# Kernel tuning notes

Measured on AMD Instinct MI355X. Metric: run time of the kernel, lower is better.

Reference implementation:

```python
import jax, jax.numpy as jnp
import numpy as np

D = 512  # input_channels
K = 64   # centers_num


def setup_inputs() -> dict:
    key = jax.random.key(0)
    k1, k2, k3, k4 = jax.random.split(key, 4)
    inputs = jax.random.normal(k1, (32, D, 56, 56), dtype=jnp.float32)
    # conv 1x1 weight/bias (nn.Conv2d(input_channels, centers_num, (1,1)))
    conv_w = jax.random.normal(k2, (K, D), dtype=jnp.float32) * (1.0 / np.sqrt(D))
    conv_b = jax.random.normal(k3, (K,), dtype=jnp.float32) * 0.01
    # centers ~ U(-0.1, 0.1), shape [D, K]
    centers = jax.random.uniform(k4, (D, K), dtype=jnp.float32, minval=-0.1, maxval=0.1)
    return {"inputs": inputs, "conv_w": conv_w, "conv_b": conv_b, "centers": centers}


def reference(inputs, conv_w, conv_b, centers):
    B, d, H, W = inputs.shape
    N = H * W
    x = inputs.reshape(B, d, N)                      # [B,D,N]
    # 1x1 conv == per-pixel linear: logits [B,K,N]
    logits = jnp.einsum('kd,bdn->bkn', conv_w, x) + conv_b[None, :, None]
    alpha = jax.nn.softmax(logits, axis=1)           # softmax over K (dim=1)
    # vlad[b,d,k] = sum_n alpha[b,k,n] * (x[b,d,n] - centers[d,k])
    vlad = jnp.einsum('bkn,bdn->bdk', alpha, x) - centers[None] * alpha.sum(axis=2)[:, None, :]
    # intra-normalize over D (torch.norm default p=2, no eps)
    vlad = vlad / jnp.linalg.norm(vlad, axis=1, keepdims=True)
    vlad = vlad.reshape(B, d * K)
    vlad = vlad / jnp.linalg.norm(vlad, axis=1, keepdims=True)
    return vlad
```

## Files before the change

### kernel.cpp

```cpp
#include <hip/hip_runtime.h>
#include <math.h>


#define NN 3136
#define DD 512
#define KK 64
#define BB 32

typedef short bf16x8 __attribute__((ext_vector_type(8)));
typedef float f32x4  __attribute__((ext_vector_type(4)));

#define SEL_HI   0x05040100u
#define SEL_LO   0x07060302u
#define SEL_PACK 0x07060302u

union FragU { uint4 u; bf16x8 f; };

static __device__ inline bf16x8 frag4(unsigned a, unsigned b, unsigned c, unsigned d) {
    FragU x; x.u = make_uint4(a, b, c, d); return x.f;
}

static __device__ inline unsigned short bf16_rne(float f) {
    unsigned u = __float_as_uint(f);
    return (unsigned short)((u + 0x7FFFu + ((u >> 16) & 1u)) >> 16);
}

__global__ __launch_bounds__(256) void wprep_kernel(
    const float* __restrict__ w, unsigned short* __restrict__ wh,
    unsigned short* __restrict__ wl, float* __restrict__ asum,
    float* __restrict__ vlad)
{
    const int i = blockIdx.x * 256 + threadIdx.x;
    if (i < 32768) {
        float v = w[i];
        float hif = __uint_as_float(__float_as_uint(v) & 0xFFFF0000u);
        float lof = v - hif;
        wh[i] = (unsigned short)(__float_as_uint(v) >> 16);
        wl[i] = (unsigned short)(__float_as_uint(lof) >> 16);
    }
    *(float4*)&vlad[(size_t)i * 4] = make_float4(0.f, 0.f, 0.f, 0.f);
    if (i < 2048) asum[i] = 0.f;
}

__global__ __launch_bounds__(256, 4) void fused_vlad(
    const float* __restrict__ x,
    const unsigned short* __restrict__ wh,
    const unsigned short* __restrict__ wl,
    const float* __restrict__ bias,
    float* __restrict__ asum,
    float* __restrict__ vlad)
{
    const int b  = blockIdx.y;
    const int n0 = blockIdx.x * 128;
    const int t  = threadIdx.x;
    const int lane = t & 63;
    const int wv   = t >> 6;
    const int c = lane & 15;
    const int q = lane >> 4;

    __shared__ __align__(16) unsigned xs_raw[128 * 36];
    __shared__ __align__(16) unsigned short wsh[64][40];
    __shared__ __align__(16) unsigned short wsl[64][40];
    unsigned short* as_ = (unsigned short*)xs_raw;

    f32x4 acc[4][2];
    #pragma unroll
    for (int mt = 0; mt < 4; mt++)
        #pragma unroll
        for (int r = 0; r < 4; r++) {
            float bv = bias[mt * 16 + q * 4 + r];
            acc[mt][0][r] = bv; acc[mt][1][r] = bv;
        }

    const float* xb = x + (size_t)b * DD * NN;
    const int n4 = t & 31;
    const int dr = t >> 5;
    const int wrow = t >> 2, wc8 = t & 3;

    float xr[16];
    uint4 wrh, wrl;
    {
        #pragma unroll
        for (int j = 0; j < 4; j++) {
            int nn = n0 + n4 + 32 * j;
            if (nn > NN - 1) nn = NN - 1;
            #pragma unroll
            for (int p = 0; p < 4; p++)
                xr[j * 4 + p] = xb[(size_t)(dr * 4 + p) * NN + nn];
        }
        wrh = *(const uint4*)&wh[(size_t)wrow * DD + wc8 * 8];
        wrl = *(const uint4*)&wl[(size_t)wrow * DD + wc8 * 8];
    }

    for (int dc = 0; dc < 16; dc++) {
        uint4 xp[4];
        #pragma unroll
        for (int j = 0; j < 4; j++) {
            unsigned pk[4];
            #pragma unroll
            for (int p = 0; p < 4; p++) {
                float v = xr[j * 4 + p];
                float hif = __uint_as_float(__float_as_uint(v) & 0xFFFF0000u);
                float lof = v - hif;
                pk[p] = __builtin_amdgcn_perm(__float_as_uint(lof), __float_as_uint(v), SEL_PACK);
            }
            xp[j] = make_uint4(pk[0], pk[1], pk[2], pk[3]);
        }
        uint4 wch = wrh, wcl = wrl;

        if (dc < 15) {
            const int d0 = (dc + 1) * 32;
            #pragma unroll
            for (int j = 0; j < 4; j++) {
                int nn = n0 + n4 + 32 * j;
                if (nn > NN - 1) nn = NN - 1;
                #pragma unroll
                for (int p = 0; p < 4; p++)
                    xr[j * 4 + p] = xb[(size_t)(d0 + dr * 4 + p) * NN + nn];
            }
            wrh = *(const uint4*)&wh[(size_t)wrow * DD + d0 + wc8 * 8];
            wrl = *(const uint4*)&wl[(size_t)wrow * DD + d0 + wc8 * 8];
        }

        __syncthreads();
        #pragma unroll
        for (int j = 0; j < 4; j++)
            *(uint4*)&xs_raw[(n4 + 32 * j) * 36 + dr * 4] = xp[j];
        *(uint4*)&wsh[wrow][wc8 * 8] = wch;
        *(uint4*)&wsl[wrow][wc8 * 8] = wcl;
        __syncthreads();

        bf16x8 ah[4], al[4], bh[2], bl[2];
        #pragma unroll
        for (int mt = 0; mt < 4; mt++) {
            ah[mt] = *(const bf16x8*)&wsh[mt * 16 + c][q * 8];
            al[mt] = *(const bf16x8*)&wsl[mt * 16 + c][q * 8];
        }
        #pragma unroll
        for (int nt = 0; nt < 2; nt++) {
            const int row = wv * 32 + nt * 16 + c;
            uint4 p0 = *(const uint4*)&xs_raw[row * 36 + q * 8];
            uint4 p1 = *(const uint4*)&xs_raw[row * 36 + q * 8 + 4];
            bh[nt] = frag4(__builtin_amdgcn_perm(p0.y, p0.x, SEL_HI),
                           __builtin_amdgcn_perm(p0.w, p0.z, SEL_HI),
                           __builtin_amdgcn_perm(p1.y, p1.x, SEL_HI),
                           __builtin_amdgcn_perm(p1.w, p1.z, SEL_HI));
            bl[nt] = frag4(__builtin_amdgcn_perm(p0.y, p0.x, SEL_LO),
                           __builtin_amdgcn_perm(p0.w, p0.z, SEL_LO),
                           __builtin_amdgcn_perm(p1.y, p1.x, SEL_LO),
                           __builtin_amdgcn_perm(p1.w, p1.z, SEL_LO));
        }
        #pragma unroll
        for (int mt = 0; mt < 4; mt++)
            #pragma unroll
            for (int nt = 0; nt < 2; nt++) {
                acc[mt][nt] = __builtin_amdgcn_mfma_f32_16x16x32_bf16(ah[mt], bh[nt], acc[mt][nt], 0, 0, 0);
                acc[mt][nt] = __builtin_amdgcn_mfma_f32_16x16x32_bf16(ah[mt], bl[nt], acc[mt][nt], 0, 0, 0);
                acc[mt][nt] = __builtin_amdgcn_mfma_f32_16x16x32_bf16(al[mt], bh[nt], acc[mt][nt], 0, 0, 0);
            }
    }

    __syncthreads();

    float sa[4][4];
    #pragma unroll
    for (int mt = 0; mt < 4; mt++)
        #pragma unroll
        for (int r = 0; r < 4; r++) sa[mt][r] = 0.f;

    #pragma unroll
    for (int nt = 0; nt < 2; nt++) {
        float mx = -1e30f;
        #pragma unroll
        for (int mt = 0; mt < 4; mt++)
            #pragma unroll
            for (int r = 0; r < 4; r++) mx = fmaxf(mx, acc[mt][nt][r]);
        mx = fmaxf(mx, __shfl_xor(mx, 16));
        mx = fmaxf(mx, __shfl_xor(mx, 32));
        float s = 0.f;
        #pragma unroll
        for (int mt = 0; mt < 4; mt++)
            #pragma unroll
            for (int r = 0; r < 4; r++) {
                float e = __expf(acc[mt][nt][r] - mx);
                acc[mt][nt][r] = e; s += e;
            }
        s += __shfl_xor(s, 16);
        s += __shfl_xor(s, 32);
        const float rinv = 1.0f / s;
        const int nloc = wv * 32 + nt * 16 + c;
        const bool ok = (n0 + nloc) < NN;
        #pragma unroll
        for (int mt = 0; mt < 4; mt++)
            #pragma unroll
            for (int r = 0; r < 4; r++) {
                unsigned short ub = bf16_rne(acc[mt][nt][r] * rinv);
                if (!ok) ub = 0;
                as_[(mt * 16 + q * 4 + r) * 136 + nloc] = ub;
                if (ok) sa[mt][r] += __uint_as_float((unsigned)ub << 16);
            }
    }
    #pragma unroll
    for (int off = 1; off <= 8; off <<= 1)
        #pragma unroll
        for (int mt = 0; mt < 4; mt++)
            #pragma unroll
            for (int r = 0; r < 4; r++)
                sa[mt][r] += __shfl_xor(sa[mt][r], off);
    if (c == 0) {
        #pragma unroll
        for (int mt = 0; mt < 4; mt++)
            #pragma unroll
            for (int r = 0; r < 4; r++)
                atomicAdd(&asum[b * KK + mt * 16 + q * 4 + r], sa[mt][r]);
    }

    __syncthreads();

    const float* xw = x + ((size_t)b * DD + wv * 128) * NN;
    float* pvb = vlad + ((size_t)b * DD + wv * 128) * KK;

    #pragma unroll
    for (int dh = 0; dh < 2; dh++) {
        f32x4 acc2[4][4];
        #pragma unroll
        for (int dt = 0; dt < 4; dt++)
            #pragma unroll
            for (int kt = 0; kt < 4; kt++)
                #pragma unroll
                for (int r = 0; r < 4; r++) acc2[dt][kt][r] = 0.f;

        #pragma unroll
        for (int ns = 0; ns < 4; ns++) {
            int nn = n0 + ns * 32 + q * 8;
            if (nn > NN - 8) nn = NN - 8;
            float4 xv[4][2];
            #pragma unroll
            for (int dt = 0; dt < 4; dt++) {
                const size_t ro = (size_t)(dh * 64 + dt * 16 + c) * NN;
                xv[dt][0] = *(const float4*)&xw[ro + nn];
                xv[dt][1] = *(const float4*)&xw[ro + nn + 4];
            }
            bf16x8 bfr[4];
            #pragma unroll
            for (int kt = 0; kt < 4; kt++)
                bfr[kt] = *(const bf16x8*)&as_[(kt * 16 + c) * 136 + ns * 32 + q * 8];
            #pragma unroll
            for (int dt = 0; dt < 4; dt++) {
                const float4 va = xv[dt][0], vb2 = xv[dt][1];
                unsigned ux = __float_as_uint(va.x),  uy = __float_as_uint(va.y);
                unsigned uz = __float_as_uint(va.z),  uw = __float_as_uint(va.w);
                unsigned vx = __float_as_uint(vb2.x), vy = __float_as_uint(vb2.y);
                unsigned vz = __float_as_uint(vb2.z), vw = __float_as_uint(vb2.w);
                bf16x8 ah = frag4(__builtin_amdgcn_perm(uy, ux, SEL_LO),
                                  __builtin_amdgcn_perm(uw, uz, SEL_LO),
                                  __builtin_amdgcn_perm(vy, vx, SEL_LO),
                                  __builtin_amdgcn_perm(vw, vz, SEL_LO));
                float lax = va.x - __uint_as_float(ux & 0xFFFF0000u);
                float lay = va.y - __uint_as_float(uy & 0xFFFF0000u);
                float laz = va.z - __uint_as_float(uz & 0xFFFF0000u);
                float law = va.w - __uint_as_float(uw & 0xFFFF0000u);
                float lbx = vb2.x - __uint_as_float(vx & 0xFFFF0000u);
                float lby = vb2.y - __uint_as_float(vy & 0xFFFF0000u);
                float lbz = vb2.z - __uint_as_float(vz & 0xFFFF0000u);
                float lbw = vb2.w - __uint_as_float(vw & 0xFFFF0000u);
                bf16x8 al2 = frag4(
                    __builtin_amdgcn_perm(__float_as_uint(lay), __float_as_uint(lax), SEL_LO),
                    __builtin_amdgcn_perm(__float_as_uint(law), __float_as_uint(laz), SEL_LO),
                    __builtin_amdgcn_perm(__float_as_uint(lby), __float_as_uint(lbx), SEL_LO),
                    __builtin_amdgcn_perm(__float_as_uint(lbw), __float_as_uint(lbz), SEL_LO));
                #pragma unroll
                for (int kt = 0; kt < 4; kt++) {
                    acc2[dt][kt] = __builtin_amdgcn_mfma_f32_16x16x32_bf16(ah,  bfr[kt], acc2[dt][kt], 0, 0, 0);
                    acc2[dt][kt] = __builtin_amdgcn_mfma_f32_16x16x32_bf16(al2, bfr[kt], acc2[dt][kt], 0, 0, 0);
                }
            }
        }
        #pragma unroll
        for (int dt = 0; dt < 4; dt++)
            #pragma unroll
            for (int r = 0; r < 4; r++) {
                const size_t dl = (size_t)(dh * 64 + dt * 16 + q * 4 + r) * KK;
                #pragma unroll
                for (int kt = 0; kt < 4; kt++)
                    atomicAdd(&pvb[dl + kt * 16 + c], acc2[dt][kt][r]);
            }
    }
}

__global__ __launch_bounds__(256) void combine_norm(
    const float* __restrict__ centers, const float* __restrict__ asum,
    float* __restrict__ vlad, float* __restrict__ psq)
{
    const int dchunk = blockIdx.x;
    const int b = blockIdx.y;
    const int t = threadIdx.x;
    const int k4 = (t & 15) * 4;
    const int dq = t >> 4;
    const float4 av = *(const float4*)&asum[b * KK + k4];
    float sqx = 0.f, sqy = 0.f, sqz = 0.f, sqw = 0.f;
    for (int i = 0; i < 8; i++) {
        const int d = dchunk * 128 + i * 16 + dq;
        const size_t idx = ((size_t)b * DD + d) * KK + k4;
        float4 p = *(const float4*)&vlad[idx];
        const float4 cv = *(const float4*)&centers[d * KK + k4];
        float vx = p.x - cv.x * av.x, vy = p.y - cv.y * av.y;
        float vz = p.z - cv.z * av.z, vw = p.w - cv.w * av.w;
        *(float4*)&vlad[idx] = make_float4(vx, vy, vz, vw);
        sqx = fmaf(vx, vx, sqx); sqy = fmaf(vy, vy, sqy);
        sqz = fmaf(vz, vz, sqz); sqw = fmaf(vw, vw, sqw);
    }
    __shared__ float red[16][64];
    red[dq][k4 + 0] = sqx; red[dq][k4 + 1] = sqy;
    red[dq][k4 + 2] = sqz; red[dq][k4 + 3] = sqw;
    __syncthreads();
    if (t < 64) {
        float s = 0.f;
        #pragma unroll
        for (int qq = 0; qq < 16; qq++) s += red[qq][t];
        psq[(b * 4 + dchunk) * 64 + t] = s;
    }
}

__global__ __launch_bounds__(256) void finalize_kernel(
    const float* __restrict__ psq, const float* __restrict__ vlad,
    float* __restrict__ out)
{
    const int dchunk = blockIdx.x;
    const int b = blockIdx.y;
    const int t = threadIdx.x;
    __shared__ float cn[64];
    if (t < 64) {
        float s = psq[b * 256 + t] + psq[b * 256 + 64 + t]
                + psq[b * 256 + 128 + t] + psq[b * 256 + 192 + t];
        cn[t] = 1.0f / (sqrtf(s) * 8.0f);
    }
    __syncthreads();
    const int k4 = (t & 15) * 4;
    const int dq = t >> 4;
    const float4 cv = *(const float4*)&cn[k4];
    #pragma unroll
    for (int i = 0; i < 8; i++) {
        const size_t idx = ((size_t)b * DD + dchunk * 128 + i * 16 + dq) * KK + k4;
        float4 v = *(const float4*)&vlad[idx];
        *(float4*)&out[idx] = make_float4(v.x * cv.x, v.y * cv.y, v.z * cv.z, v.w * cv.w);
    }
}

extern "C" void kernel_launch(void* const* d_in, const int* in_sizes, int n_in,
                              void* d_out, int out_size, void* d_ws, size_t ws_size,
                              hipStream_t stream) {
    const float* x       = (const float*)d_in[0];
    const float* conv_w  = (const float*)d_in[1];
    const float* conv_b  = (const float*)d_in[2];
    const float* centers = (const float*)d_in[3];
    float* out = (float*)d_out;

    unsigned short* wh = (unsigned short*)d_ws;
    unsigned short* wl = wh + 32768;
    float* asum = (float*)(wl + 32768);
    float* vlad = asum + 2048;
    float* psq  = vlad + 1048576;

    wprep_kernel   <<<dim3(1024),    dim3(256), 0, stream>>>(conv_w, wh, wl, asum, vlad);
    fused_vlad     <<<dim3(25, BB),  dim3(256), 0, stream>>>(x, wh, wl, conv_b, asum, vlad);
    combine_norm   <<<dim3(4, BB),   dim3(256), 0, stream>>>(centers, asum, vlad, psq);
    finalize_kernel<<<dim3(4, BB),   dim3(256), 0, stream>>>(psq, vlad, out);
}
```

Measured before the change: 408.1 us.

## Restage second GEMM through shared memory with per-wave K split and prefetch

The second phase (alpha^T x accumulation) now loads x cooperatively into registers, converts each value to packed hi/lo bf16 once, and stages it in shared memory in 32-row D chunks. Each wave owns one 16-wide K slice and loops over all D chunks, with the next chunk's global loads prefetched during the current compute. Before, each wave loaded its own D rows straight from global memory and split them into hi/lo per k-tile. The change aims to make the global loads coalesced and cut the conversion work, at the cost of two barriers per chunk, more, smaller atomic-add rounds, and less MFMA work per LDS read.

New measurement: 406.9 us. About the same (-0.3%).

```diff
diff --git a/kernel.cpp b/kernel.cpp
--- a/kernel.cpp
+++ b/kernel.cpp
@@ -58,10 +58,12 @@
     const int c = lane & 15;
     const int q = lane >> 4;
 
-    __shared__ __align__(16) unsigned xs_raw[128 * 36];
-    __shared__ __align__(16) unsigned short wsh[64][40];
-    __shared__ __align__(16) unsigned short wsl[64][40];
-    unsigned short* as_ = (unsigned short*)xs_raw;
+    __shared__ __align__(16) unsigned char smem[28672];
+    unsigned*       xs_raw = (unsigned*)smem;
+    unsigned short* wsh    = (unsigned short*)(smem + 18432);
+    unsigned short* wsl    = (unsigned short*)(smem + 23552);
+    unsigned short* as_    = (unsigned short*)smem;
+    unsigned*       xs2    = (unsigned*)smem;
 
     f32x4 acc[4][2];
     #pragma unroll
@@ -126,15 +128,15 @@
         #pragma unroll
         for (int j = 0; j < 4; j++)
             *(uint4*)&xs_raw[(n4 + 32 * j) * 36 + dr * 4] = xp[j];
-        *(uint4*)&wsh[wrow][wc8 * 8] = wch;
-        *(uint4*)&wsl[wrow][wc8 * 8] = wcl;
+        *(uint4*)&wsh[wrow * 40 + wc8 * 8] = wch;
+        *(uint4*)&wsl[wrow * 40 + wc8 * 8] = wcl;
         __syncthreads();
 
         bf16x8 ah[4], al[4], bh[2], bl[2];
         #pragma unroll
         for (int mt = 0; mt < 4; mt++) {
-            ah[mt] = *(const bf16x8*)&wsh[mt * 16 + c][q * 8];
-            al[mt] = *(const bf16x8*)&wsl[mt * 16 + c][q * 8];
+            ah[mt] = *(const bf16x8*)&wsh[(mt * 16 + c) * 40 + q * 8];
+            al[mt] = *(const bf16x8*)&wsl[(mt * 16 + c) * 40 + q * 8];
         }
         #pragma unroll
         for (int nt = 0; nt < 2; nt++) {
@@ -162,6 +164,17 @@
 
     __syncthreads();
 
+    const int sr = t >> 4;
+    const int sc = (t & 15) * 8;
+    int ncol = n0 + sc; if (ncol > NN - 8) ncol = NN - 8;
+    float4 sxr[2][2];
+    #pragma unroll
+    for (int i = 0; i < 2; i++) {
+        const size_t ro = (size_t)(i * 16 + sr) * NN;
+        sxr[i][0] = *(const float4*)&xb[ro + ncol];
+        sxr[i][1] = *(const float4*)&xb[ro + ncol + 4];
+    }
+
     float sa[4][4];
     #pragma unroll
     for (int mt = 0; mt < 4; mt++)
@@ -217,73 +230,76 @@
 
     __syncthreads();
 
-    const float* xw = x + ((size_t)b * DD + wv * 128) * NN;
-    float* pvb = vlad + ((size_t)b * DD + wv * 128) * KK;
-
-    #pragma unroll
-    for (int dh = 0; dh < 2; dh++) {
-        f32x4 acc2[4][4];
-        #pragma unroll
-        for (int dt = 0; dt < 4; dt++)
-            #pragma unroll
-            for (int kt = 0; kt < 4; kt++)
-                #pragma unroll
-                for (int r = 0; r < 4; r++) acc2[dt][kt][r] = 0.f;
+    bf16x8 bfr[4];
+    #pragma unroll
+    for (int ns = 0; ns < 4; ns++)
+        bfr[ns] = *(const bf16x8*)&as_[(wv * 16 + c) * 136 + ns * 32 + q * 8];
+
+    float* pvb = vlad + (size_t)b * DD * KK + wv * 16;
+
+    for (int ch = 0; ch < 16; ch++) {
+        unsigned pk[2][8];
+        #pragma unroll
+        for (int i = 0; i < 2; i++) {
+            const float vv[8] = { sxr[i][0].x, sxr[i][0].y, sxr[i][0].z, sxr[i][0].w,
+                                  sxr[i][1].x, sxr[i][1].y, sxr[i][1].z, sxr[i][1].w };
+            #pragma unroll
+            for (int j = 0; j < 8; j++) {
+                unsigned u = __float_as_uint(vv[j]);
+                float lo = vv[j] - __uint_as_float(u & 0xFFFF0000u);
+                pk[i][j] = __builtin_amdgcn_perm(__float_as_uint(lo), u, SEL_PACK);
+            }
+        }
+        if (ch < 15) {
+            const size_t dbase = (size_t)(ch + 1) * 32;
+            #pragma unroll
+            for (int i = 0; i < 2; i++) {
+                const size_t ro = (dbase + i * 16 + sr) * NN;
+                sxr[i][0] = *(const float4*)&xb[ro + ncol];
+                sxr[i][1] = *(const float4*)&xb[ro + ncol + 4];
+            }
+        }
+
+        __syncthreads();
+        #pragma unroll
+        for (int i = 0; i < 2; i++) {
+            *(uint4*)&xs2[(i * 16 + sr) * 132 + sc]     = make_uint4(pk[i][0], pk[i][1], pk[i][2], pk[i][3]);
+            *(uint4*)&xs2[(i * 16 + sr) * 132 + sc + 4] = make_uint4(pk[i][4], pk[i][5], pk[i][6], pk[i][7]);
+        }
+        __syncthreads();
+
+        f32x4 a2[2];
+        #pragma unroll
+        for (int dt = 0; dt < 2; dt++)
+            #pragma unroll
+            for (int r = 0; r < 4; r++) a2[dt][r] = 0.f;
 
         #pragma unroll
         for (int ns = 0; ns < 4; ns++) {
-            int nn = n0 + ns * 32 + q * 8;
-            if (nn > NN - 8) nn = NN - 8;
-            float4 xv[4][2];
-            #pragma unroll
-            for (int dt = 0; dt < 4; dt++) {
-                const size_t ro = (size_t)(dh * 64 + dt * 16 + c) * NN;
-                xv[dt][0] = *(const float4*)&xw[ro + nn];
-                xv[dt][1] = *(const float4*)&xw[ro + nn + 4];
-            }
-            bf16x8 bfr[4];
-            #pragma unroll
-            for (int kt = 0; kt < 4; kt++)
-                bfr[kt] = *(const bf16x8*)&as_[(kt * 16 + c) * 136 + ns * 32 + q * 8];
-            #pragma unroll
-            for (int dt = 0; dt < 4; dt++) {
-                const float4 va = xv[dt][0], vb2 = xv[dt][1];
-                unsigned ux = __float_as_uint(va.x),  uy = __float_as_uint(va.y);
-                unsigned uz = __float_as_uint(va.z),  uw = __float_as_uint(va.w);
-                unsigned vx = __float_as_uint(vb2.x), vy = __float_as_uint(vb2.y);
-                unsigned vz = __float_as_uint(vb2.z), vw = __float_as_uint(vb2.w);
-                bf16x8 ah = frag4(__builtin_amdgcn_perm(uy, ux, SEL_LO),
-                                  __builtin_amdgcn_perm(uw, uz, SEL_LO),
-                                  __builtin_amdgcn_perm(vy, vx, SEL_LO),
-                                  __builtin_amdgcn_perm(vw, vz, SEL_LO));
-                float lax = va.x - __uint_as_float(ux & 0xFFFF0000u);
-                float lay = va.y - __uint_as_float(uy & 0xFFFF0000u);
-                float laz = va.z - __uint_as_float(uz & 0xFFFF0000u);
-                float law = va.w - __uint_as_float(uw & 0xFFFF0000u);
-                float lbx = vb2.x - __uint_as_float(vx & 0xFFFF0000u);
-                float lby = vb2.y - __uint_as_float(vy & 0xFFFF0000u);
-                float lbz = vb2.z - __uint_as_float(vz & 0xFFFF0000u);
-                float lbw = vb2.w - __uint_as_float(vw & 0xFFFF0000u);
-                bf16x8 al2 = frag4(
-                    __builtin_amdgcn_perm(__float_as_uint(lay), __float_as_uint(lax), SEL_LO),
-                    __builtin_amdgcn_perm(__float_as_uint(law), __float_as_uint(laz), SEL_LO),
-                    __builtin_amdgcn_perm(__float_as_uint(lby), __float_as_uint(lbx), SEL_LO),
-                    __builtin_amdgcn_perm(__float_as_uint(lbw), __float_as_uint(lbz), SEL_LO));
-                #pragma unroll
-                for (int kt = 0; kt < 4; kt++) {
-                    acc2[dt][kt] = __builtin_amdgcn_mfma_f32_16x16x32_bf16(ah,  bfr[kt], acc2[dt][kt], 0, 0, 0);
-                    acc2[dt][kt] = __builtin_amdgcn_mfma_f32_16x16x32_bf16(al2, bfr[kt], acc2[dt][kt], 0, 0, 0);
-                }
-            }
-        }
-        #pragma unroll
-        for (int dt = 0; dt < 4; dt++)
+            #pragma unroll
+            for (int dt = 0; dt < 2; dt++) {
+                const int base = (dt * 16 + c) * 132 + ns * 32 + q * 8;
+                uint4 p0 = *(const uint4*)&xs2[base];
+                uint4 p1 = *(const uint4*)&xs2[base + 4];
+                bf16x8 ah = frag4(__builtin_amdgcn_perm(p0.y, p0.x, SEL_HI),
+                                  __builtin_amdgcn_perm(p0.w, p0.z, SEL_HI),
+                                  __builtin_amdgcn_perm(p1.y, p1.x, SEL_HI),
+                                  __builtin_amdgcn_perm(p1.w, p1.z, SEL_HI));
+                bf16x8 al2 = frag4(__builtin_amdgcn_perm(p0.y, p0.x, SEL_LO),
+                                   __builtin_amdgcn_perm(p0.w, p0.z, SEL_LO),
+                                   __builtin_amdgcn_perm(p1.y, p1.x, SEL_LO),
+                                   __builtin_amdgcn_perm(p1.w, p1.z, SEL_LO));
+                a2[dt] = __builtin_amdgcn_mfma_f32_16x16x32_bf16(ah,  bfr[ns], a2[dt], 0, 0, 0);
+                a2[dt] = __builtin_amdgcn_mfma_f32_16x16x32_bf16(al2, bfr[ns], a2[dt], 0, 0, 0);
+            }
+        }
+
+        #pragma unroll
+        for (int dt = 0; dt < 2; dt++)
             #pragma unroll
             for (int r = 0; r < 4; r++) {
-                const size_t dl = (size_t)(dh * 64 + dt * 16 + q * 4 + r) * KK;
-                #pragma unroll
-                for (int kt = 0; kt < 4; kt++)
-                    atomicAdd(&pvb[dl + kt * 16 + c], acc2[dt][kt][r]);
+                const int d = ch * 32 + dt * 16 + q * 4 + r;
+                atomicAdd(&pvb[(size_t)d * KK + c], a2[dt][r]);
             }
     }
 }
```
